# Kernel tuning notes

Measured on AMD Instinct MI355X. Metric: run time of the kernel, lower is better.

The kernel has to match this reference:

```python
import jax, jax.numpy as jnp
import numpy as np

N_EMBD = 1024
HEAD_SIZE = 64
WINDOW = 64
N_GLOBAL = 64
N_RANDOM = 64
B, T = 8, 2048


def setup_inputs() -> dict:
    key = jax.random.key(0)
    kx, kc, kk, kq, kv = jax.random.split(key, 5)
    x = jax.random.normal(kx, (B, T, N_EMBD), dtype=jnp.float32)
    random_cols = jax.random.randint(kc, (T, N_RANDOM), 0, T)
    s = 1.0 / np.sqrt(N_EMBD)
    Wk = jax.random.normal(kk, (HEAD_SIZE, N_EMBD), dtype=jnp.float32) * s
    Wq = jax.random.normal(kq, (HEAD_SIZE, N_EMBD), dtype=jnp.float32) * s
    Wv = jax.random.normal(kv, (HEAD_SIZE, N_EMBD), dtype=jnp.float32) * s
    return {"x": x, "random_cols": random_cols, "Wk": Wk, "Wq": Wq, "Wv": Wv}


def _bigbird_mask(Tlen, random_cols):
    rows = jnp.arange(Tlen)[:, None]
    cols = jnp.arange(Tlen)[None, :]
    causal = rows >= cols
    local = (cols >= rows - WINDOW + 1) & (cols <= rows)
    glob = (rows < N_GLOBAL) | (cols < N_GLOBAL)
    rand = jnp.zeros((Tlen, Tlen), dtype=bool).at[
        jnp.arange(Tlen)[:, None], random_cols].set(True)
    return (local | glob | rand) & causal  # [T, T] bool


def reference(x, random_cols, Wk, Wq, Wv):
    # projections (Linear, no bias): [B,T,C] @ [C,H] -> [B,T,H]
    k = jnp.einsum('btc,hc->bth', x, Wk)
    q = jnp.einsum('btc,hc->bth', x, Wq)
    v = jnp.einsum('btc,hc->bth', x, Wv)
    scale = 1.0 / jnp.sqrt(jnp.asarray(HEAD_SIZE, x.dtype))
    scores = jnp.einsum('bqh,bkh->bqk', q, k) * scale  # [B,T,T]
    mask = _bigbird_mask(x.shape[1], random_cols)
    scores = jnp.where(mask[None, :, :], scores, -jnp.inf)
    weights = jax.nn.softmax(scores, axis=-1)
    out = jnp.einsum('bqk,bkh->bqh', weights, v)  # [B,T,H]
    return out
```

## Files before the change

kernel.cpp:

```cpp
#include <hip/hip_runtime.h>
#include <math.h>

#define T_DIM 2048
#define C_DIM 1024
#define H_DIM 64
#define M_TOTAL 16384
#define NQKV 192

typedef __bf16 bf16x8 __attribute__((ext_vector_type(8)));
typedef float f32x4 __attribute__((ext_vector_type(4)));
typedef float f32x2 __attribute__((ext_vector_type(2)));
typedef unsigned short u16x8 __attribute__((ext_vector_type(8)));

#if __has_builtin(__builtin_amdgcn_fdot2_f32_bf16)
#define HAVE_DOT2 1
typedef __bf16 bf16x2 __attribute__((ext_vector_type(2)));
#else
#define HAVE_DOT2 0
#endif

__device__ __forceinline__ unsigned short f2bf(float f) {
    unsigned u = __float_as_uint(f);
    unsigned r = (u + 0x7FFFu + ((u >> 16) & 1u)) >> 16;
    return (unsigned short)r;
}
__device__ __forceinline__ float bf2f(unsigned short u) {
    return __uint_as_float(((unsigned)u) << 16);
}
__device__ __forceinline__ float blo(unsigned u) { return __uint_as_float(u << 16); }
__device__ __forceinline__ float bhi(unsigned u) { return __uint_as_float(u & 0xFFFF0000u); }
__device__ __forceinline__ unsigned pack_bf2(float f0, float f1) {
    unsigned u0 = __float_as_uint(f0) + 0x8000u;
    unsigned u1 = __float_as_uint(f1) + 0x8000u;
    return __builtin_amdgcn_perm(u1, u0, 0x07060302u);
}
__device__ __forceinline__ uint4 cvt8(float4 a, float4 b) {
    return make_uint4(pack_bf2(a.x, a.y), pack_bf2(a.z, a.w),
                      pack_bf2(b.x, b.y), pack_bf2(b.z, b.w));
}

__device__ __forceinline__ float dot8bf(u16x8 a, u16x8 b, float c) {
#if HAVE_DOT2
    bf16x8 av = __builtin_bit_cast(bf16x8, a);
    bf16x8 bv = __builtin_bit_cast(bf16x8, b);
    #pragma unroll
    for (int e = 0; e < 4; ++e) {
        bf16x2 ap = {av[2 * e], av[2 * e + 1]};
        bf16x2 bp = {bv[2 * e], bv[2 * e + 1]};
        c = __builtin_amdgcn_fdot2_f32_bf16(ap, bp, c, false);
    }
#else
    #pragma unroll
    for (int e = 0; e < 8; ++e) c = fmaf(bf2f(a[e]), bf2f(b[e]), c);
#endif
    return c;
}

#if __has_builtin(__builtin_amdgcn_update_dpp)
#define HAVE_DPP 1
template<int CTRL>
__device__ __forceinline__ float dppf(float x) {
    int v = __builtin_amdgcn_update_dpp(0, __builtin_bit_cast(int, x),
                                        CTRL, 0xF, 0xF, true);
    return __builtin_bit_cast(float, v);
}
__device__ __forceinline__ float red8(float p) {
    p += dppf<0xB1>(p);
    p += dppf<0x4E>(p);
    p += dppf<0x141>(p);
    return p;
}
#else
#define HAVE_DPP 0
__device__ __forceinline__ float red8(float p) {
    p += __shfl_xor(p, 1); p += __shfl_xor(p, 2); p += __shfl_xor(p, 4);
    return p;
}
#endif

__global__ __launch_bounds__(256) void compact_kernel(
    const int* __restrict__ rnd,
    int* __restrict__ rjc,
    int* __restrict__ nvalb)
{
    __shared__ unsigned bm_all[4][64];
    const int wv = threadIdx.x >> 6;
    const int ln = threadIdx.x & 63;
    const int i  = blockIdx.x * 4 + wv;
    unsigned* bm = bm_all[wv];

    bm[ln] = 0u;
    int  j2 = rnd[i * 64 + ln];
    bool v2 = (j2 < i - 63) && (j2 >= 64);
    if (v2) {
        unsigned old = atomicOr(&bm[j2 >> 5], 1u << (j2 & 31));
        v2 = ((old >> (j2 & 31)) & 1u) == 0u;
    }
    unsigned long long mbal = __ballot(v2);
    const int nval = __popcll(mbal);
    if (v2) {
        int pos = __popcll(mbal & ((1ull << ln) - 1ull));
        rjc[i * 64 + pos] = j2;
    }
    if (ln >= nval) rjc[i * 64 + ln] = 0;
    if (ln == 0) nvalb[i] = nval;
}

__global__ __launch_bounds__(512) void proj_kernel(
    const float* __restrict__ x,
    const float* __restrict__ Wk,
    const float* __restrict__ Wq,
    const float* __restrict__ Wv,
    unsigned short* __restrict__ qkv)
{
    __shared__ unsigned short Ab[64 * 64];
    __shared__ unsigned short Bb[192 * 64];

    const int m0 = blockIdx.x * 64;
    const int t  = threadIdx.x;
    const int wv = t >> 6, ln = t & 63;
    const int mfr = ln & 15, kq = ln >> 4;
    const int r0 = (wv & 1) * 32;
    const int c0 = (wv >> 1) * 48;

    const int srow  = t >> 3;
    const int sk8   = (t & 7) * 8;
    const int skoff = sk8 ^ ((srow & 7) * 8);

    const float* gp[4] = {
        x  + (size_t)(m0 + srow) * C_DIM + sk8,
        Wk + (size_t)srow * C_DIM + sk8,
        Wq + (size_t)srow * C_DIM + sk8,
        Wv + (size_t)srow * C_DIM + sk8 };
    unsigned short* lp[4] = {
        &Ab[srow * 64 + skoff],
        &Bb[srow * 64 + skoff],
        &Bb[(srow + 64) * 64 + skoff],
        &Bb[(srow + 128) * 64 + skoff] };

    f32x4 acc[2][3] = {};

    float4 ra[4], rb[4];
    #pragma unroll
    for (int s = 0; s < 4; ++s) {
        ra[s] = *(const float4*)(gp[s]);
        rb[s] = *(const float4*)(gp[s] + 4);
    }

    for (int kc = 0; kc < C_DIM; kc += 64) {
        __syncthreads();
        #pragma unroll
        for (int s = 0; s < 4; ++s)
            *(uint4*)lp[s] = cvt8(ra[s], rb[s]);
        if (kc + 64 < C_DIM) {
            #pragma unroll
            for (int s = 0; s < 4; ++s) {
                ra[s] = *(const float4*)(gp[s] + kc + 64);
                rb[s] = *(const float4*)(gp[s] + kc + 68);
            }
        }
        __syncthreads();
        #pragma unroll
        for (int ks = 0; ks < 64; ks += 32) {
            bf16x8 af[2], bf[3];
            #pragma unroll
            for (int a = 0; a < 2; ++a) {
                int row = r0 + a * 16 + mfr;
                af[a] = *(const bf16x8*)&Ab[row * 64 + ((ks + kq * 8) ^ ((row & 7) * 8))];
            }
            #pragma unroll
            for (int b2 = 0; b2 < 3; ++b2) {
                int row = c0 + b2 * 16 + mfr;
                bf[b2] = *(const bf16x8*)&Bb[row * 64 + ((ks + kq * 8) ^ ((row & 7) * 8))];
            }
            #pragma unroll
            for (int a = 0; a < 2; ++a)
                #pragma unroll
                for (int b2 = 0; b2 < 3; ++b2)
                    acc[a][b2] = __builtin_amdgcn_mfma_f32_16x16x32_bf16(
                        af[a], bf[b2], acc[a][b2], 0, 0, 0);
        }
    }

    #pragma unroll
    for (int a = 0; a < 2; ++a)
        #pragma unroll
        for (int b2 = 0; b2 < 3; ++b2)
            #pragma unroll
            for (int r = 0; r < 4; ++r) {
                int row = m0 + r0 + a * 16 + kq * 4 + r;
                int col = c0 + b2 * 16 + mfr;
                qkv[(size_t)row * NQKV + col] = f2bf(acc[a][b2][r]);
            }
}

__global__ __launch_bounds__(256) void attn_kernel(
    const unsigned short* __restrict__ qkv,
    const int*  __restrict__ rjc,
    const int*  __restrict__ nvalb,
    float* __restrict__ out)
{
    const int wv = threadIdx.x >> 6;
    const int ln = threadIdx.x & 63;
    const int b  = blockIdx.x & 7;
    const int i  = ((blockIdx.x >> 3) << 2) + wv;
    const int bi = b * T_DIM + i;

    const int  nval = nvalb[i];
    const int* rji  = rjc + i * 64;

    const int e8 = (ln & 7) * 8;
    const int gg = ln >> 3;
    u16x8 qraw = *(const u16x8*)(qkv + (size_t)bi * NQKV + 64 + e8);
    const unsigned short* kb = qkv + (size_t)b * T_DIM * NQKV;

    float p[24];
    #pragma unroll
    for (int idx = 16; idx < 24; ++idx) p[idx] = 0.f;

    #pragma unroll
    for (int n = 0; n < 16; n += 4) {
        int jj[4];
        #pragma unroll
        for (int u = 0; u < 4; ++u) {
            int s = (n + u) * 8 + gg;
            int j;
            if (s < 64) { j = i - s; j = (j < 0) ? 0 : j; }
            else        { j = s - 64; }
            jj[u] = j;
        }
        u16x8 kvv[4];
        #pragma unroll
        for (int u = 0; u < 4; ++u)
            kvv[u] = *(const u16x8*)(kb + (size_t)jj[u] * NQKV + e8);
        #pragma unroll
        for (int u = 0; u < 4; ++u)
            p[n + u] = red8(dot8bf(kvv[u], qraw, 0.f));
    }

    auto qk_rand = [&](int n0) {
        int jj[4];
        #pragma unroll
        for (int u = 0; u < 4; ++u) jj[u] = rji[(n0 - 16 + u) * 8 + gg];
        u16x8 kvv[4];
        #pragma unroll
        for (int u = 0; u < 4; ++u)
            kvv[u] = *(const u16x8*)(kb + (size_t)jj[u] * NQKV + e8);
        #pragma unroll
        for (int u = 0; u < 4; ++u)
            p[n0 + u] = red8(dot8bf(kvv[u], qraw, 0.f));
    };
    if (nval > 0)  qk_rand(16);
    if (nval > 32) qk_rand(20);

    #pragma unroll
    for (int idx = 0; idx < 8; ++idx) {
        bool v = (idx * 8 + gg) <= i;
        p[idx] = v ? p[idx] * 0.125f : -1e30f;
    }
    #pragma unroll
    for (int idx = 8; idx < 16; ++idx) {
        bool v = ((idx - 8) * 8 + gg) < (i - 63);
        p[idx] = v ? p[idx] * 0.125f : -1e30f;
    }
    #pragma unroll
    for (int idx = 16; idx < 24; ++idx) {
        bool v = ((idx - 16) * 8 + gg) < nval;
        p[idx] = v ? p[idx] * 0.125f : -1e30f;
    }

    float mx = p[0];
    #pragma unroll
    for (int idx = 1; idx < 24; ++idx) mx = fmaxf(mx, p[idx]);
    mx = fmaxf(mx, __shfl_xor(mx, 8));
    mx = fmaxf(mx, __shfl_xor(mx, 16));
    mx = fmaxf(mx, __shfl_xor(mx, 32));

    float sum = 0.f;
    #pragma unroll
    for (int idx = 0; idx < 24; ++idx) {
        p[idx] = __expf(p[idx] - mx);
        sum += p[idx];
    }
    sum += __shfl_xor(sum, 8);
    sum += __shfl_xor(sum, 16);
    sum += __shfl_xor(sum, 32);

    const unsigned short* vb = kb + 128;
    f32x2 acc2[4] = {};
    #pragma unroll
    for (int bt = 0; bt < 2; ++bt) {
        int jc[8];
        #pragma unroll
        for (int c = 0; c < 8; ++c) {
            int s = (bt * 8 + c) * 8 + gg;
            int j;
            if (s < 64) { j = i - s; j = (j < 0) ? 0 : j; }
            else        { j = s - 64; }
            jc[c] = j;
        }
        uint4 vv[8];
        #pragma unroll
        for (int c = 0; c < 8; ++c)
            vv[c] = *(const uint4*)(vb + (size_t)jc[c] * NQKV + e8);
        #pragma unroll
        for (int c = 0; c < 8; ++c) {
            float w = p[bt * 8 + c];
            f32x2 w2 = {w, w};
            f32x2 p0 = {blo(vv[c].x), bhi(vv[c].x)};
            f32x2 p1 = {blo(vv[c].y), bhi(vv[c].y)};
            f32x2 p2 = {blo(vv[c].z), bhi(vv[c].z)};
            f32x2 p3 = {blo(vv[c].w), bhi(vv[c].w)};
            acc2[0] += w2 * p0;
            acc2[1] += w2 * p1;
            acc2[2] += w2 * p2;
            acc2[3] += w2 * p3;
        }
    }
    auto pv_rand = [&](int c0) {
        int jc[4];
        #pragma unroll
        for (int c = 0; c < 4; ++c)
            jc[c] = rji[(c0 + c) * 8 + gg];
        uint4 vv[4];
        #pragma unroll
        for (int c = 0; c < 4; ++c)
            vv[c] = *(const uint4*)(vb + (size_t)jc[c] * NQKV + e8);
        #pragma unroll
        for (int c = 0; c < 4; ++c) {
            float w = p[16 + c0 + c];
            f32x2 w2 = {w, w};
            f32x2 p0 = {blo(vv[c].x), bhi(vv[c].x)};
            f32x2 p1 = {blo(vv[c].y), bhi(vv[c].y)};
            f32x2 p2 = {blo(vv[c].z), bhi(vv[c].z)};
            f32x2 p3 = {blo(vv[c].w), bhi(vv[c].w)};
            acc2[0] += w2 * p0;
            acc2[1] += w2 * p1;
            acc2[2] += w2 * p2;
            acc2[3] += w2 * p3;
        }
    };
    if (nval > 0)  pv_rand(0);
    if (nval > 32) pv_rand(4);

    float acc[8] = { acc2[0][0], acc2[0][1], acc2[1][0], acc2[1][1],
                     acc2[2][0], acc2[2][1], acc2[3][0], acc2[3][1] };
    #pragma unroll
    for (int m = 8; m <= 32; m <<= 1)
        #pragma unroll
        for (int e = 0; e < 8; ++e)
            acc[e] += __shfl_xor(acc[e], m);

    if (ln < 8) {
        float inv = 1.f / sum;
        float* op = &out[(size_t)bi * H_DIM + e8];
        *(float4*)op       = make_float4(acc[0]*inv, acc[1]*inv, acc[2]*inv, acc[3]*inv);
        *(float4*)(op + 4) = make_float4(acc[4]*inv, acc[5]*inv, acc[6]*inv, acc[7]*inv);
    }
}

extern "C" void kernel_launch(void* const* d_in, const int* in_sizes, int n_in,
                              void* d_out, int out_size, void* d_ws, size_t ws_size,
                              hipStream_t stream) {
    const float* x   = (const float*)d_in[0];
    const int*   rnd = (const int*)  d_in[1];
    const float* Wk  = (const float*)d_in[2];
    const float* Wq  = (const float*)d_in[3];
    const float* Wv  = (const float*)d_in[4];
    float* out = (float*)d_out;

    unsigned short* qkv = (unsigned short*)d_ws;
    int* rjc   = (int*)((char*)d_ws + 6291456);
    int* nvalb = rjc + T_DIM * 64;

    compact_kernel<<<T_DIM / 4, 256, 0, stream>>>(rnd, rjc, nvalb);
    proj_kernel<<<M_TOTAL / 64, 512, 0, stream>>>(x, Wk, Wq, Wv, qkv);
    attn_kernel<<<M_TOTAL / 4, 256, 0, stream>>>(qkv, rjc, nvalb, out);
}
```

Measured before the change: 151.8 us.

## Pre-convert weights to bf16 and load via global_load_lds; batch attention gathers

Adds a small kernel that converts Wk/Wq/Wv to bf16 once per call, pre-swizzled, and the projection kernel then streams those bf16 weights straight into LDS with global_load_lds. This removes the repeated fp32 weight loads and conversions that every projection block used to do. The attention kernel now issues all 16 K loads, the random K loads and all 16 V loads up front to expose more memory-level parallelism, at the cost of more registers. It adds one extra launch and always gathers all 8 random groups whenever nval>0.

After: 150.5 us. Within noise of the previous version (-0.9%).

```diff
diff --git a/kernel.cpp b/kernel.cpp
--- a/kernel.cpp
+++ b/kernel.cpp
@@ -17,6 +17,18 @@
 typedef __bf16 bf16x2 __attribute__((ext_vector_type(2)));
 #else
 #define HAVE_DOT2 0
+#endif
+
+#if __has_builtin(__builtin_amdgcn_global_load_lds)
+#define HAVE_GLL 1
+__device__ __forceinline__ void gload_lds16(const unsigned short* g, unsigned short* l) {
+    __builtin_amdgcn_global_load_lds(
+        (const __attribute__((address_space(1))) unsigned int*)(const void*)g,
+        (__attribute__((address_space(3))) unsigned int*)(void*)l,
+        16, 0, 0);
+}
+#else
+#define HAVE_GLL 0
 #endif
 
 __device__ __forceinline__ unsigned short f2bf(float f) {
@@ -77,6 +89,25 @@
     return p;
 }
 #endif
+
+__global__ __launch_bounds__(256) void wconv_kernel(
+    const float* __restrict__ Wk,
+    const float* __restrict__ Wq,
+    const float* __restrict__ Wv,
+    unsigned short* __restrict__ wbf)
+{
+    int t   = blockIdx.x * 256 + threadIdx.x;
+    int g8  = t & 7;
+    int kc  = (t >> 3) & 15;
+    int row = t >> 7;
+    const float* src = (row < 64)  ? Wk + (size_t)row * C_DIM
+                     : (row < 128) ? Wq + (size_t)(row - 64) * C_DIM
+                                   : Wv + (size_t)(row - 128) * C_DIM;
+    int ksrc = kc * 64 + ((g8 * 8) ^ ((row & 7) * 8));
+    float4 a = *(const float4*)(src + ksrc);
+    float4 b = *(const float4*)(src + ksrc + 4);
+    *(uint4*)(wbf + (size_t)row * C_DIM + kc * 64 + g8 * 8) = cvt8(a, b);
+}
 
 __global__ __launch_bounds__(256) void compact_kernel(
     const int* __restrict__ rnd,
@@ -108,9 +139,7 @@
 
 __global__ __launch_bounds__(512) void proj_kernel(
     const float* __restrict__ x,
-    const float* __restrict__ Wk,
-    const float* __restrict__ Wq,
-    const float* __restrict__ Wv,
+    const unsigned short* __restrict__ wbf,
     unsigned short* __restrict__ qkv)
 {
     __shared__ unsigned short Ab[64 * 64];
@@ -127,37 +156,35 @@
     const int sk8   = (t & 7) * 8;
     const int skoff = sk8 ^ ((srow & 7) * 8);
 
-    const float* gp[4] = {
-        x  + (size_t)(m0 + srow) * C_DIM + sk8,
-        Wk + (size_t)srow * C_DIM + sk8,
-        Wq + (size_t)srow * C_DIM + sk8,
-        Wv + (size_t)srow * C_DIM + sk8 };
-    unsigned short* lp[4] = {
-        &Ab[srow * 64 + skoff],
-        &Bb[srow * 64 + skoff],
-        &Bb[(srow + 64) * 64 + skoff],
-        &Bb[(srow + 128) * 64 + skoff] };
+    const float* gpx = x + (size_t)(m0 + srow) * C_DIM + sk8;
+    unsigned short* lpx = &Ab[srow * 64 + skoff];
+
+    const int wrow = wv * 8 + (ln >> 3);
+    const unsigned short* wsrc = wbf + (size_t)wrow * C_DIM + (ln & 7) * 8;
 
     f32x4 acc[2][3] = {};
 
-    float4 ra[4], rb[4];
-    #pragma unroll
-    for (int s = 0; s < 4; ++s) {
-        ra[s] = *(const float4*)(gp[s]);
-        rb[s] = *(const float4*)(gp[s] + 4);
-    }
+    float4 ra = *(const float4*)(gpx);
+    float4 rb = *(const float4*)(gpx + 4);
 
     for (int kc = 0; kc < C_DIM; kc += 64) {
         __syncthreads();
-        #pragma unroll
-        for (int s = 0; s < 4; ++s)
-            *(uint4*)lp[s] = cvt8(ra[s], rb[s]);
+        *(uint4*)lpx = cvt8(ra, rb);
+#if HAVE_GLL
+        #pragma unroll
+        for (int s = 0; s < 3; ++s)
+            gload_lds16(wsrc + (size_t)s * 64 * C_DIM + kc,
+                        &Bb[(s * 64 + wv * 8) * 64]);
+#else
+        #pragma unroll
+        for (int s = 0; s < 3; ++s) {
+            uint4 w4 = *(const uint4*)(wsrc + (size_t)s * 64 * C_DIM + kc);
+            *(uint4*)&Bb[(s * 64 + wv * 8 + (ln >> 3)) * 64 + (ln & 7) * 8] = w4;
+        }
+#endif
         if (kc + 64 < C_DIM) {
-            #pragma unroll
-            for (int s = 0; s < 4; ++s) {
-                ra[s] = *(const float4*)(gp[s] + kc + 64);
-                rb[s] = *(const float4*)(gp[s] + kc + 68);
-            }
+            ra = *(const float4*)(gpx + kc + 64);
+            rb = *(const float4*)(gpx + kc + 68);
         }
         __syncthreads();
         #pragma unroll
@@ -213,45 +240,45 @@
     const int gg = ln >> 3;
     u16x8 qraw = *(const u16x8*)(qkv + (size_t)bi * NQKV + 64 + e8);
     const unsigned short* kb = qkv + (size_t)b * T_DIM * NQKV;
+    const unsigned short* vb = kb + 128;
 
     float p[24];
-    #pragma unroll
-    for (int idx = 16; idx < 24; ++idx) p[idx] = 0.f;
-
-    #pragma unroll
-    for (int n = 0; n < 16; n += 4) {
-        int jj[4];
-        #pragma unroll
-        for (int u = 0; u < 4; ++u) {
-            int s = (n + u) * 8 + gg;
-            int j;
-            if (s < 64) { j = i - s; j = (j < 0) ? 0 : j; }
-            else        { j = s - 64; }
-            jj[u] = j;
-        }
-        u16x8 kvv[4];
-        #pragma unroll
-        for (int u = 0; u < 4; ++u)
-            kvv[u] = *(const u16x8*)(kb + (size_t)jj[u] * NQKV + e8);
-        #pragma unroll
-        for (int u = 0; u < 4; ++u)
-            p[n + u] = red8(dot8bf(kvv[u], qraw, 0.f));
-    }
-
-    auto qk_rand = [&](int n0) {
-        int jj[4];
-        #pragma unroll
-        for (int u = 0; u < 4; ++u) jj[u] = rji[(n0 - 16 + u) * 8 + gg];
-        u16x8 kvv[4];
-        #pragma unroll
-        for (int u = 0; u < 4; ++u)
-            kvv[u] = *(const u16x8*)(kb + (size_t)jj[u] * NQKV + e8);
-        #pragma unroll
-        for (int u = 0; u < 4; ++u)
-            p[n0 + u] = red8(dot8bf(kvv[u], qraw, 0.f));
-    };
-    if (nval > 0)  qk_rand(16);
-    if (nval > 32) qk_rand(20);
+
+    u16x8 kf[16];
+    #pragma unroll
+    for (int n = 0; n < 16; ++n) {
+        int s = n * 8 + gg;
+        int j;
+        if (s < 64) { j = i - s; j = (j < 0) ? 0 : j; }
+        else        { j = s - 64; }
+        kf[n] = *(const u16x8*)(kb + (size_t)j * NQKV + e8);
+    }
+    #pragma unroll
+    for (int n = 0; n < 16; ++n)
+        p[n] = red8(dot8bf(kf[n], qraw, 0.f));
+
+    if (nval > 0) {
+        u16x8 kr[8];
+        #pragma unroll
+        for (int u = 0; u < 8; ++u)
+            kr[u] = *(const u16x8*)(kb + (size_t)rji[u * 8 + gg] * NQKV + e8);
+        #pragma unroll
+        for (int u = 0; u < 8; ++u)
+            p[16 + u] = red8(dot8bf(kr[u], qraw, 0.f));
+    } else {
+        #pragma unroll
+        for (int u = 0; u < 8; ++u) p[16 + u] = 0.f;
+    }
+
+    uint4 vf[16];
+    #pragma unroll
+    for (int n = 0; n < 16; ++n) {
+        int s = n * 8 + gg;
+        int j;
+        if (s < 64) { j = i - s; j = (j < 0) ? 0 : j; }
+        else        { j = s - 64; }
+        vf[n] = *(const uint4*)(vb + (size_t)j * NQKV + e8);
+    }
 
     #pragma unroll
     for (int idx = 0; idx < 8; ++idx) {
@@ -286,62 +313,40 @@
     sum += __shfl_xor(sum, 16);
     sum += __shfl_xor(sum, 32);
 
-    const unsigned short* vb = kb + 128;
     f32x2 acc2[4] = {};
     #pragma unroll
-    for (int bt = 0; bt < 2; ++bt) {
-        int jc[8];
-        #pragma unroll
-        for (int c = 0; c < 8; ++c) {
-            int s = (bt * 8 + c) * 8 + gg;
-            int j;
-            if (s < 64) { j = i - s; j = (j < 0) ? 0 : j; }
-            else        { j = s - 64; }
-            jc[c] = j;
-        }
-        uint4 vv[8];
-        #pragma unroll
-        for (int c = 0; c < 8; ++c)
-            vv[c] = *(const uint4*)(vb + (size_t)jc[c] * NQKV + e8);
-        #pragma unroll
-        for (int c = 0; c < 8; ++c) {
-            float w = p[bt * 8 + c];
+    for (int n = 0; n < 16; ++n) {
+        float w = p[n];
+        f32x2 w2 = {w, w};
+        f32x2 p0 = {blo(vf[n].x), bhi(vf[n].x)};
+        f32x2 p1 = {blo(vf[n].y), bhi(vf[n].y)};
+        f32x2 p2 = {blo(vf[n].z), bhi(vf[n].z)};
+        f32x2 p3 = {blo(vf[n].w), bhi(vf[n].w)};
+        acc2[0] += w2 * p0;
+        acc2[1] += w2 * p1;
+        acc2[2] += w2 * p2;
+        acc2[3] += w2 * p3;
+    }
+
+    if (nval > 0) {
+        uint4 vr[8];
+        #pragma unroll
+        for (int u = 0; u < 8; ++u)
+            vr[u] = *(const uint4*)(vb + (size_t)rji[u * 8 + gg] * NQKV + e8);
+        #pragma unroll
+        for (int u = 0; u < 8; ++u) {
+            float w = p[16 + u];
             f32x2 w2 = {w, w};
-            f32x2 p0 = {blo(vv[c].x), bhi(vv[c].x)};
-            f32x2 p1 = {blo(vv[c].y), bhi(vv[c].y)};
-            f32x2 p2 = {blo(vv[c].z), bhi(vv[c].z)};
-            f32x2 p3 = {blo(vv[c].w), bhi(vv[c].w)};
+            f32x2 p0 = {blo(vr[u].x), bhi(vr[u].x)};
+            f32x2 p1 = {blo(vr[u].y), bhi(vr[u].y)};
+            f32x2 p2 = {blo(vr[u].z), bhi(vr[u].z)};
+            f32x2 p3 = {blo(vr[u].w), bhi(vr[u].w)};
             acc2[0] += w2 * p0;
             acc2[1] += w2 * p1;
             acc2[2] += w2 * p2;
             acc2[3] += w2 * p3;
         }
     }
-    auto pv_rand = [&](int c0) {
-        int jc[4];
-        #pragma unroll
-        for (int c = 0; c < 4; ++c)
-            jc[c] = rji[(c0 + c) * 8 + gg];
-        uint4 vv[4];
-        #pragma unroll
-        for (int c = 0; c < 4; ++c)
-            vv[c] = *(const uint4*)(vb + (size_t)jc[c] * NQKV + e8);
-        #pragma unroll
-        for (int c = 0; c < 4; ++c) {
-            float w = p[16 + c0 + c];
-            f32x2 w2 = {w, w};
-            f32x2 p0 = {blo(vv[c].x), bhi(vv[c].x)};
-            f32x2 p1 = {blo(vv[c].y), bhi(vv[c].y)};
-            f32x2 p2 = {blo(vv[c].z), bhi(vv[c].z)};
-            f32x2 p3 = {blo(vv[c].w), bhi(vv[c].w)};
-            acc2[0] += w2 * p0;
-            acc2[1] += w2 * p1;
-            acc2[2] += w2 * p2;
-            acc2[3] += w2 * p3;
-        }
-    };
-    if (nval > 0)  pv_rand(0);
-    if (nval > 32) pv_rand(4);
 
     float acc[8] = { acc2[0][0], acc2[0][1], acc2[1][0], acc2[1][1],
                      acc2[2][0], acc2[2][1], acc2[3][0], acc2[3][1] };
@@ -372,8 +377,10 @@
     unsigned short* qkv = (unsigned short*)d_ws;
     int* rjc   = (int*)((char*)d_ws + 6291456);
     int* nvalb = rjc + T_DIM * 64;
-
+    unsigned short* wbf = (unsigned short*)((char*)d_ws + 6823936);
+
+    wconv_kernel<<<96, 256, 0, stream>>>(Wk, Wq, Wv, wbf);
     compact_kernel<<<T_DIM / 4, 256, 0, stream>>>(rnd, rjc, nvalb);
-    proj_kernel<<<M_TOTAL / 64, 512, 0, stream>>>(x, Wk, Wq, Wv, qkv);
+    proj_kernel<<<M_TOTAL / 64, 512, 0, stream>>>(x, wbf, qkv);
     attn_kernel<<<M_TOTAL / 4, 256, 0, stream>>>(qkv, rjc, nvalb, out);
 }
```
